# Kernel optimization log

Measured on AMD Instinct MI355X. Metric: run time of the kernel, lower is better.

Reference implementation:

```python
import jax, jax.numpy as jnp
import numpy as np


def conv1x1(x, w, b):
    # x: [B, Cin, H, W], w: [Cout, Cin], b: [Cout]
    return jnp.einsum('oc,bchw->bohw', w, x) + b[None, :, None, None]


def setup_inputs() -> dict:
    key = jax.random.key(0)
    ks = jax.random.split(key, 10)
    B, C, H, W = 8, 256, 64, 64
    C2 = C // 2
    s = 1.0 / np.sqrt(C)
    s2 = 1.0 / np.sqrt(C2)
    return {
        'x1': jax.random.normal(ks[0], (B, C, H, W), jnp.float32),
        'x2': jax.random.normal(ks[1], (B, C, H, W), jnp.float32),
        'w_th': jax.random.uniform(ks[2], (C2, C), jnp.float32, -s, s),
        'b_th': jax.random.uniform(ks[3], (C2,), jnp.float32, -s, s),
        'w_pi': jax.random.uniform(ks[4], (C2, C), jnp.float32, -s, s),
        'b_pi': jax.random.uniform(ks[5], (C2,), jnp.float32, -s, s),
        'w_g': jax.random.uniform(ks[6], (C2, C), jnp.float32, -s, s),
        'b_g': jax.random.uniform(ks[7], (C2,), jnp.float32, -s, s),
        'w_out': jax.random.uniform(ks[8], (C, C2), jnp.float32, -s2, s2),
        'b_out': jax.random.uniform(ks[9], (C,), jnp.float32, -s2, s2),
    }


def reference(x1, x2, w_th, b_th, w_pi, b_pi, w_g, b_g, w_out, b_out):
    B, C, H, W = x1.shape
    HW = H * W
    res = x1
    # 1x1 conv projections -> [B, C2, HW]
    e1 = conv1x1(x1, w_th, b_th).reshape(B, -1, HW)  # theta
    e2 = conv1x1(x2, w_pi, b_pi).reshape(B, -1, HW)  # phi
    # scores: [B, HW, HW]
    f = jnp.einsum('bcq,bck->bqk', e1, e2)
    # GLOBAL softmax over the whole HWxHW matrix per batch element
    f = jax.nn.softmax(f.reshape(B, HW * HW), axis=1).reshape(B, HW, HW)
    g2 = conv1x1(x2, w_g, b_g).reshape(B, -1, HW)  # [B, C2, HW]
    # out = f @ g2^T -> [B, HW, C2] -> [B, C2, H, W]
    out = jnp.einsum('bqk,bck->bcq', f, g2).reshape(B, -1, H, W)
    out = conv1x1(out, w_out, b_out)
    return out + res
```

## Files before the change

kernel.cpp:

```cpp
#include <hip/hip_runtime.h>

typedef unsigned short u16;
typedef unsigned int u32;
typedef short s16x8 __attribute__((ext_vector_type(8)));
typedef float f32x4 __attribute__((ext_vector_type(4)));

#define HWN 4096
#define CC  256
#define C2  128

static __device__ __forceinline__ u16 f2bf(float f) {
    union { float f; u32 u; } c; c.f = f;
    u32 u = c.u;
    u32 r = (u + 0x7fffu + ((u >> 16) & 1u)) >> 16;
    return (u16)r;
}
static __device__ __forceinline__ float bf2f(u16 u) {
    union { u32 u; float f; } c; c.u = ((u32)u) << 16; return c.f;
}
static __device__ __forceinline__ u32 cvtpk(float lo, float hi) {
    u32 d;
    asm("v_cvt_pk_bf16_f32 %0, %1, %2" : "=v"(d) : "v"(lo), "v"(hi));
    return d;
}

__global__ __launch_bounds__(256) void k_wcvt(
    const float* __restrict__ w_th, const float* __restrict__ w_pi,
    const float* __restrict__ w_g,  const float* __restrict__ w_out,
    u16* __restrict__ wthb, u16* __restrict__ wpib,
    u16* __restrict__ wgb,  u16* __restrict__ woutb)
{
    int i = blockIdx.x * 256 + threadIdx.x;
    wthb[i]  = f2bf(w_th[i]);
    wpib[i]  = f2bf(w_pi[i]);
    wgb[i]   = f2bf(w_g[i]);
    woutb[i] = f2bf(w_out[i]);
}

__device__ __forceinline__ void load_afrag(const float* __restrict__ px, int g, s16x8 a[8]) {
    #pragma unroll
    for (int ks = 0; ks < 8; ++ks) {
        union { s16x8 v; u16 u[8]; } c;
        #pragma unroll
        for (int j = 0; j < 8; ++j)
            c.u[j] = f2bf(px[(size_t)(ks*32 + g*8 + j) * HWN]);
        a[ks] = c.v;
    }
}

__device__ __forceinline__ void proj_gemm(const s16x8 a[8], const u16* __restrict__ wb,
                                          const float* __restrict__ bias,
                                          int m16, int g, f32x4 acc[8]) {
    #pragma unroll
    for (int nb = 0; nb < 8; ++nb) {
        float bv = bias[nb*16 + m16];
        acc[nb] = (f32x4){bv, bv, bv, bv};
    }
    #pragma unroll
    for (int ks = 0; ks < 8; ++ks) {
        #pragma unroll
        for (int nb = 0; nb < 8; ++nb) {
            s16x8 bb = *(const s16x8*)&wb[(size_t)(nb*16 + m16)*CC + ks*32 + g*8];
            acc[nb] = __builtin_amdgcn_mfma_f32_16x16x32_bf16(a[ks], bb, acc[nb], 0, 0, 0);
        }
    }
}

__global__ __launch_bounds__(256) void k_projM(
    const float* __restrict__ x1, const float* __restrict__ x2,
    const u16* __restrict__ wthb, const float* __restrict__ b_th,
    const u16* __restrict__ wpib, const float* __restrict__ b_pi,
    const u16* __restrict__ wgb,  const float* __restrict__ b_g,
    u16* __restrict__ e1t, u16* __restrict__ e2t, u16* __restrict__ g2c)
{
    __shared__ u16 gs[C2][72];
    const int tid  = threadIdx.x;
    const int b    = blockIdx.x >> 6;
    const int q0   = (blockIdx.x & 63) * 64;
    const int wid  = __builtin_amdgcn_readfirstlane(tid >> 6);
    const int lane = tid & 63;
    const int m16  = lane & 15;
    const int g    = lane >> 4;

    s16x8 a[8];
    f32x4 acc[8];

    const float* px1 = x1 + (size_t)b*CC*HWN + q0 + wid*16 + m16;
    load_afrag(px1, g, a);
    proj_gemm(a, wthb, b_th, m16, g, acc);
    #pragma unroll
    for (int nb = 0; nb < 8; ++nb)
        #pragma unroll
        for (int r = 0; r < 4; ++r)
            e1t[((size_t)b*HWN + q0 + wid*16 + g*4 + r)*C2 + nb*16 + m16] = f2bf(acc[nb][r]);

    const float* px2 = x2 + (size_t)b*CC*HWN + q0 + wid*16 + m16;
    load_afrag(px2, g, a);
    proj_gemm(a, wpib, b_pi, m16, g, acc);
    #pragma unroll
    for (int nb = 0; nb < 8; ++nb)
        #pragma unroll
        for (int r = 0; r < 4; ++r)
            e2t[((size_t)b*HWN + q0 + wid*16 + g*4 + r)*C2 + nb*16 + m16] = f2bf(acc[nb][r]);

    proj_gemm(a, wgb, b_g, m16, g, acc);
    #pragma unroll
    for (int nb = 0; nb < 8; ++nb)
        #pragma unroll
        for (int r = 0; r < 4; ++r)
            gs[nb*16 + m16][wid*16 + g*4 + r] = f2bf(acc[nb][r]);
    __syncthreads();
    #pragma unroll
    for (int r = 0; r < 4; ++r) {
        int idx = r*256 + tid;
        int c2 = idx >> 3, q8 = idx & 7;
        union { u16 u[8]; int4 v; } o;
        #pragma unroll
        for (int e = 0; e < 8; ++e) {
            int kp = q8*8 + e;
            int kk = kp >> 5, rem = kp & 31;
            int gg = rem >> 3, jj = rem & 7;
            int ko = kk*32 + ((jj >> 2) << 4) + (gg << 2) + (jj & 3);
            o.u[e] = gs[c2][ko];
        }
        *(int4*)&g2c[((size_t)b*C2 + c2)*HWN + q0 + q8*8] = o.v;
    }
}

__global__ __launch_bounds__(256, 2) void k_flash(
    const u16* __restrict__ e1t, const u16* __restrict__ e2t,
    const u16* __restrict__ g2c,
    u16* __restrict__ outp0, u16* __restrict__ outp1, float* __restrict__ ms)
{
    __shared__ u16 e2s[64*128];
    __shared__ u16 g2s[128*64];

    const int tid  = threadIdx.x;
    const int bid  = ((blockIdx.x & 7) << 6) | (blockIdx.x >> 3);
    const int b    = bid >> 6;
    const int qb   = (bid >> 1) & 31;
    const int seg  = bid & 1;
    const int q0   = qb * 128;
    const int wid  = __builtin_amdgcn_readfirstlane(tid >> 6);
    const int lane = tid & 63;
    const int m16  = lane & 15;
    const int g    = lane >> 4;
    const int sw16 = (m16 & 7) << 3;

    s16x8 af[2][4];
    #pragma unroll
    for (int h = 0; h < 2; ++h) {
        const u16* p = e1t + ((size_t)b*HWN + q0 + wid*32 + h*16 + m16)*C2 + g*8;
        #pragma unroll
        for (int kc = 0; kc < 4; ++kc) af[h][kc] = *(const s16x8*)(p + kc*32);
    }

    f32x4 acc[2][8];
    #pragma unroll
    for (int h = 0; h < 2; ++h)
        #pragma unroll
        for (int i = 0; i < 8; ++i) acc[h][i] = (f32x4){0.f,0.f,0.f,0.f};
    float m_w = -INFINITY, s_w = 0.f;

    const u16* e2base = e2t + (size_t)b*HWN*C2;
    const u16* g2base = g2c + (size_t)b*C2*HWN;
    const int er = tid >> 4, ec = tid & 15;
    const int gr = tid >> 3, gc = tid & 7;

    for (int it = 0; it < 32; ++it) {
        const int k0 = seg*2048 + it*64;
        __syncthreads();
        #pragma unroll
        for (int r = 0; r < 4; ++r) {
            int row = r*16 + er;
            int4 v = *(const int4*)(e2base + (size_t)(k0 + row)*C2 + ec*8);
            *(int4*)&e2s[(row*128 + ec*8) ^ ((row & 7) << 3)] = v;
        }
        #pragma unroll
        for (int r = 0; r < 4; ++r) {
            int row = r*32 + gr;
            int4 v = *(const int4*)(g2base + (size_t)row*HWN + k0 + gc*8);
            *(int4*)&g2s[(row*64 + gc*8) ^ ((row & 7) << 3)] = v;
        }
        __syncthreads();

        f32x4 s[2][4];
        #pragma unroll
        for (int h = 0; h < 2; ++h)
            #pragma unroll
            for (int j = 0; j < 4; ++j) s[h][j] = (f32x4){0.f,0.f,0.f,0.f};
        #pragma unroll
        for (int j = 0; j < 4; ++j) {
            #pragma unroll
            for (int kc = 0; kc < 4; ++kc) {
                s16x8 aa = *(const s16x8*)&e2s[((j*16+m16)*128 + kc*32 + g*8) ^ sw16];
                s[0][j] = __builtin_amdgcn_mfma_f32_16x16x32_bf16(aa, af[0][kc], s[0][j], 0, 0, 0);
                s[1][j] = __builtin_amdgcn_mfma_f32_16x16x32_bf16(aa, af[1][kc], s[1][j], 0, 0, 0);
            }
        }

        float tm = -INFINITY;
        #pragma unroll
        for (int h = 0; h < 2; ++h)
            #pragma unroll
            for (int j = 0; j < 4; ++j)
                #pragma unroll
                for (int r = 0; r < 4; ++r) tm = fmaxf(tm, s[h][j][r]);
        #pragma unroll
        for (int off = 32; off >= 1; off >>= 1) tm = fmaxf(tm, __shfl_xor(tm, off));
        if (tm > m_w + 8.f) {
            const float sc = __expf(m_w - tm);
            s_w *= sc;
            #pragma unroll
            for (int h = 0; h < 2; ++h)
                #pragma unroll
                for (int i = 0; i < 8; ++i) {
                    acc[h][i][0] *= sc; acc[h][i][1] *= sc;
                    acc[h][i][2] *= sc; acc[h][i][3] *= sc;
                }
            m_w = tm;
        }
        float psum = 0.f;
        u32 w[2][4][2];
        #pragma unroll
        for (int h = 0; h < 2; ++h)
            #pragma unroll
            for (int j = 0; j < 4; ++j) {
                float p0 = __expf(s[h][j][0] - m_w);
                float p1 = __expf(s[h][j][1] - m_w);
                float p2 = __expf(s[h][j][2] - m_w);
                float p3 = __expf(s[h][j][3] - m_w);
                psum += (p0 + p1) + (p2 + p3);
                w[h][j][0] = cvtpk(p0, p1);
                w[h][j][1] = cvtpk(p2, p3);
            }
        s_w += psum;

        s16x8 pa[2][2];
        #pragma unroll
        for (int h = 0; h < 2; ++h)
            #pragma unroll
            for (int kk = 0; kk < 2; ++kk) {
                union { u32 d[4]; s16x8 v; } pf;
                pf.d[0] = w[h][2*kk][0];
                pf.d[1] = w[h][2*kk][1];
                pf.d[2] = w[h][2*kk+1][0];
                pf.d[3] = w[h][2*kk+1][1];
                pa[h][kk] = pf.v;
            }

        #pragma unroll
        for (int kk = 0; kk < 2; ++kk) {
            #pragma unroll
            for (int fc = 0; fc < 8; ++fc) {
                s16x8 gb = *(const s16x8*)&g2s[((fc*16+m16)*64 + kk*32 + g*8) ^ sw16];
                acc[0][fc] = __builtin_amdgcn_mfma_f32_16x16x32_bf16(pa[0][kk], gb, acc[0][fc], 0, 0, 0);
                acc[1][fc] = __builtin_amdgcn_mfma_f32_16x16x32_bf16(pa[1][kk], gb, acc[1][fc], 0, 0, 0);
            }
        }
    }

    #pragma unroll
    for (int off = 32; off >= 1; off >>= 1) s_w += __shfl_xor(s_w, off);
    if (lane == 0) {
        int idx = b*256 + seg*128 + qb*4 + wid;
        ms[idx*2 + 0] = m_w;
        ms[idx*2 + 1] = s_w;
    }
    const float inv_s = 1.f / s_w;
    u16* op = seg ? outp1 : outp0;
    #pragma unroll
    for (int h = 0; h < 2; ++h)
        #pragma unroll
        for (int fc = 0; fc < 8; ++fc)
            #pragma unroll
            for (int r = 0; r < 4; ++r)
                op[((size_t)b*HWN + q0 + wid*32 + h*16 + g*4 + r)*C2 + fc*16 + m16] =
                    f2bf(acc[h][fc][r] * inv_s);
}

__global__ void k_mz(const float* __restrict__ ms, float* __restrict__ mz)
{
    __shared__ float rmax[4], rsum[4];
    const int b = blockIdx.x, tid = threadIdx.x;
    const int lane = tid & 63, wid = tid >> 6;
    float m = ms[((size_t)b*256 + tid)*2 + 0];
    float s = ms[((size_t)b*256 + tid)*2 + 1];
    float mm = m;
    #pragma unroll
    for (int off = 32; off >= 1; off >>= 1) mm = fmaxf(mm, __shfl_xor(mm, off));
    if (lane == 0) rmax[wid] = mm;
    __syncthreads();
    float M = fmaxf(fmaxf(rmax[0], rmax[1]), fmaxf(rmax[2], rmax[3]));
    float z = s * __expf(m - M);
    #pragma unroll
    for (int off = 32; off >= 1; off >>= 1) z += __shfl_xor(z, off);
    if (lane == 0) rsum[wid] = z;
    __syncthreads();
    if (tid == 0) { mz[b*2] = M; mz[b*2+1] = rsum[0]+rsum[1]+rsum[2]+rsum[3]; }
}

__global__ __launch_bounds__(256) void k_outM(
    const u16* __restrict__ outp0, const u16* __restrict__ outp1,
    const float* __restrict__ ms, const float* __restrict__ mz,
    const u16* __restrict__ woutb, const float* __restrict__ b_out,
    const float* __restrict__ x1, float* __restrict__ out)
{
    const int tid  = threadIdx.x;
    const int b    = blockIdx.x >> 6;
    const int q0   = (blockIdx.x & 63) * 64;
    const int wv   = tid >> 6;
    const int lane = tid & 63;
    const int m16  = lane & 15;
    const int g    = lane >> 4;
    const int q    = q0 + wv*16 + m16;

    const float M    = mz[b*2];
    const float invZ = 1.f / mz[b*2+1];
    const int idx5   = (q0 >> 5) + (wv >> 1);
    const float a0 = ms[(b*256 + idx5)*2+1]       * __expf(ms[(b*256 + idx5)*2]       - M) * invZ;
    const float a1 = ms[(b*256 + 128 + idx5)*2+1] * __expf(ms[(b*256 + 128 + idx5)*2] - M) * invZ;

    s16x8 bfr[4];
    #pragma unroll
    for (int ks = 0; ks < 4; ++ks) {
        union { s16x8 v; u16 u[8]; } o0, o1, oc;
        o0.v = *(const s16x8*)&outp0[((size_t)b*HWN + q)*C2 + ks*32 + g*8];
        o1.v = *(const s16x8*)&outp1[((size_t)b*HWN + q)*C2 + ks*32 + g*8];
        #pragma unroll
        for (int j = 0; j < 8; ++j)
            oc.u[j] = f2bf(a0*bf2f(o0.u[j]) + a1*bf2f(o1.u[j]));
        bfr[ks] = oc.v;
    }

    f32x4 acc[16];
    #pragma unroll
    for (int cb = 0; cb < 16; ++cb) acc[cb] = (f32x4){0.f,0.f,0.f,0.f};
    #pragma unroll
    for (int ks = 0; ks < 4; ++ks) {
        #pragma unroll
        for (int cb = 0; cb < 16; ++cb) {
            s16x8 afr = *(const s16x8*)&woutb[(size_t)(cb*16 + m16)*C2 + ks*32 + g*8];
            acc[cb] = __builtin_amdgcn_mfma_f32_16x16x32_bf16(afr, bfr[ks], acc[cb], 0, 0, 0);
        }
    }

    #pragma unroll
    for (int cb = 0; cb < 16; ++cb) {
        f32x4 bb = *(const f32x4*)&b_out[cb*16 + g*4];
        #pragma unroll
        for (int r = 0; r < 4; ++r) {
            int co = cb*16 + g*4 + r;
            size_t o = ((size_t)b*CC + co)*HWN + q;
            out[o] = acc[cb][r] + bb[r] + x1[o];
        }
    }
}

extern "C" void kernel_launch(void* const* d_in, const int* in_sizes, int n_in,
                              void* d_out, int out_size, void* d_ws, size_t ws_size,
                              hipStream_t stream)
{
    const float* x1   = (const float*)d_in[0];
    const float* x2   = (const float*)d_in[1];
    const float* w_th = (const float*)d_in[2];
    const float* b_th = (const float*)d_in[3];
    const float* w_pi = (const float*)d_in[4];
    const float* b_pi = (const float*)d_in[5];
    const float* w_g  = (const float*)d_in[6];
    const float* b_g  = (const float*)d_in[7];
    const float* w_out= (const float*)d_in[8];
    const float* b_out= (const float*)d_in[9];
    float* out = (float*)d_out;

    char* ws = (char*)d_ws;
    u16*   e1t  = (u16*)(ws);
    u16*   e2t  = (u16*)(ws + 8388608);
    u16*   g2c  = (u16*)(ws + 16777216);
    u16*   outp0= (u16*)(ws + 25165824);
    u16*   outp1= (u16*)(ws + 33554432);
    float* ms   = (float*)(ws + 41943040);
    float* mz   = (float*)(ws + 41959424);
    u16*   wthb = (u16*)(ws + 41959488);
    u16*   wpib = (u16*)(ws + 42025024);
    u16*   wgb  = (u16*)(ws + 42090560);
    u16*   woutb= (u16*)(ws + 42156096);

    k_wcvt <<<dim3(128), dim3(256), 0, stream>>>(w_th, w_pi, w_g, w_out, wthb, wpib, wgb, woutb);
    k_projM<<<dim3(512), dim3(256), 0, stream>>>(x1, x2, wthb, b_th, wpib, b_pi, wgb, b_g,
                                                 e1t, e2t, g2c);
    k_flash<<<dim3(512), dim3(256), 0, stream>>>(e1t, e2t, g2c, outp0, outp1, ms);
    k_mz   <<<dim3(8),   dim3(256), 0, stream>>>(ms, mz);
    k_outM <<<dim3(512), dim3(256), 0, stream>>>(outp0, outp1, ms, mz, woutb, b_out, x1, out);
}
```

Baseline: 182.1 us.

## Double-buffer flash tiles via direct global-to-LDS loads with pre-swizzled layouts

The projection kernel now writes e2 and g2 in a pre-swizzled, tile-contiguous layout. This lets the flash kernel fetch each 64-key tile with global_load_lds straight into LDS, double-buffered so the next tile loads while the current one is computed. It also folds log2(e) into the theta weights and bias so the softmax can use exp2f instead of exp. In exchange it doubles LDS usage per block, which may limit occupancy at two blocks per CU, and it ties the flash kernel to the new layout.

```diff
diff --git a/kernel.cpp b/kernel.cpp
--- a/kernel.cpp
+++ b/kernel.cpp
@@ -8,6 +8,7 @@
 #define HWN 4096
 #define CC  256
 #define C2  128
+#define LOG2E 1.4426950408889634f
 
 static __device__ __forceinline__ u16 f2bf(float f) {
     union { float f; u32 u; } c; c.f = f;
@@ -23,6 +24,8 @@
     asm("v_cvt_pk_bf16_f32 %0, %1, %2" : "=v"(d) : "v"(lo), "v"(hi));
     return d;
 }
+#define GLB(p) ((const __attribute__((address_space(1))) void*)(p))
+#define LDS(p) ((__attribute__((address_space(3))) void*)(p))
 
 __global__ __launch_bounds__(256) void k_wcvt(
     const float* __restrict__ w_th, const float* __restrict__ w_pi,
@@ -31,7 +34,7 @@
     u16* __restrict__ wgb,  u16* __restrict__ woutb)
 {
     int i = blockIdx.x * 256 + threadIdx.x;
-    wthb[i]  = f2bf(w_th[i]);
+    wthb[i]  = f2bf(w_th[i] * LOG2E);
     wpib[i]  = f2bf(w_pi[i]);
     wgb[i]   = f2bf(w_g[i]);
     woutb[i] = f2bf(w_out[i]);
@@ -49,11 +52,11 @@
 }
 
 __device__ __forceinline__ void proj_gemm(const s16x8 a[8], const u16* __restrict__ wb,
-                                          const float* __restrict__ bias,
+                                          const float* __restrict__ bias, float bscale,
                                           int m16, int g, f32x4 acc[8]) {
     #pragma unroll
     for (int nb = 0; nb < 8; ++nb) {
-        float bv = bias[nb*16 + m16];
+        float bv = bias[nb*16 + m16] * bscale;
         acc[nb] = (f32x4){bv, bv, bv, bv};
     }
     #pragma unroll
@@ -71,7 +74,7 @@
     const u16* __restrict__ wthb, const float* __restrict__ b_th,
     const u16* __restrict__ wpib, const float* __restrict__ b_pi,
     const u16* __restrict__ wgb,  const float* __restrict__ b_g,
-    u16* __restrict__ e1t, u16* __restrict__ e2t, u16* __restrict__ g2c)
+    u16* __restrict__ e1t, u16* __restrict__ e2t, u16* __restrict__ g2t)
 {
     __shared__ u16 gs[C2][72];
     const int tid  = threadIdx.x;
@@ -87,7 +90,7 @@
 
     const float* px1 = x1 + (size_t)b*CC*HWN + q0 + wid*16 + m16;
     load_afrag(px1, g, a);
-    proj_gemm(a, wthb, b_th, m16, g, acc);
+    proj_gemm(a, wthb, b_th, LOG2E, m16, g, acc);
     #pragma unroll
     for (int nb = 0; nb < 8; ++nb)
         #pragma unroll
@@ -96,44 +99,49 @@
 
     const float* px2 = x2 + (size_t)b*CC*HWN + q0 + wid*16 + m16;
     load_afrag(px2, g, a);
-    proj_gemm(a, wpib, b_pi, m16, g, acc);
+    proj_gemm(a, wpib, b_pi, 1.f, m16, g, acc);
     #pragma unroll
     for (int nb = 0; nb < 8; ++nb)
         #pragma unroll
-        for (int r = 0; r < 4; ++r)
-            e2t[((size_t)b*HWN + q0 + wid*16 + g*4 + r)*C2 + nb*16 + m16] = f2bf(acc[nb][r]);
-
-    proj_gemm(a, wgb, b_g, m16, g, acc);
+        for (int r = 0; r < 4; ++r) {
+            int q   = q0 + wid*16 + g*4 + r;
+            int gix = (nb*2 + (m16 >> 3)) ^ (q & 7);
+            e2t[((size_t)b*HWN + q)*C2 + gix*8 + (m16 & 7)] = f2bf(acc[nb][r]);
+        }
+
+    proj_gemm(a, wgb, b_g, 1.f, m16, g, acc);
     #pragma unroll
     for (int nb = 0; nb < 8; ++nb)
         #pragma unroll
         for (int r = 0; r < 4; ++r)
             gs[nb*16 + m16][wid*16 + g*4 + r] = f2bf(acc[nb][r]);
     __syncthreads();
+    u16* gt = g2t + ((size_t)b*64 + (q0 >> 6))*8192;
     #pragma unroll
     for (int r = 0; r < 4; ++r) {
         int idx = r*256 + tid;
-        int c2 = idx >> 3, q8 = idx & 7;
+        int row = idx >> 3, c8 = idx & 7;
         union { u16 u[8]; int4 v; } o;
         #pragma unroll
         for (int e = 0; e < 8; ++e) {
-            int kp = q8*8 + e;
-            int kk = kp >> 5, rem = kp & 31;
+            int c  = c8*8 + e;
+            int cs = c ^ ((row & 7) << 3);
+            int kk = cs >> 5, rem = cs & 31;
             int gg = rem >> 3, jj = rem & 7;
             int ko = kk*32 + ((jj >> 2) << 4) + (gg << 2) + (jj & 3);
-            o.u[e] = gs[c2][ko];
-        }
-        *(int4*)&g2c[((size_t)b*C2 + c2)*HWN + q0 + q8*8] = o.v;
+            o.u[e] = gs[row][ko];
+        }
+        *(int4*)&gt[row*64 + c8*8] = o.v;
     }
 }
 
 __global__ __launch_bounds__(256, 2) void k_flash(
     const u16* __restrict__ e1t, const u16* __restrict__ e2t,
-    const u16* __restrict__ g2c,
+    const u16* __restrict__ g2t,
     u16* __restrict__ outp0, u16* __restrict__ outp1, float* __restrict__ ms)
 {
-    __shared__ u16 e2s[64*128];
-    __shared__ u16 g2s[128*64];
+    __shared__ u16 e2s[2][64*128];
+    __shared__ u16 g2s[2][128*64];
 
     const int tid  = threadIdx.x;
     const int bid  = ((blockIdx.x & 7) << 6) | (blockIdx.x >> 3);
@@ -163,26 +171,37 @@
     float m_w = -INFINITY, s_w = 0.f;
 
     const u16* e2base = e2t + (size_t)b*HWN*C2;
-    const u16* g2base = g2c + (size_t)b*C2*HWN;
-    const int er = tid >> 4, ec = tid & 15;
-    const int gr = tid >> 3, gc = tid & 7;
+    const u16* g2base = g2t + (size_t)b*64*8192;
+    const int  wof    = wid * 2048;
+    const int  lof    = lane * 8;
+
+    {
+        const u16* eG = e2base + (size_t)(seg*2048)*C2 + wof + lof;
+        const u16* gG = g2base + (size_t)(seg*32)*8192 + wof + lof;
+        u16* eL = &e2s[0][0] + wof;
+        u16* gL = &g2s[0][0] + wof;
+        #pragma unroll
+        for (int c = 0; c < 4; ++c) {
+            __builtin_amdgcn_global_load_lds(GLB(eG + c*512), LDS(eL + c*512), 16, 0, 0);
+            __builtin_amdgcn_global_load_lds(GLB(gG + c*512), LDS(gL + c*512), 16, 0, 0);
+        }
+    }
+    __syncthreads();
 
     for (int it = 0; it < 32; ++it) {
-        const int k0 = seg*2048 + it*64;
-        __syncthreads();
-        #pragma unroll
-        for (int r = 0; r < 4; ++r) {
-            int row = r*16 + er;
-            int4 v = *(const int4*)(e2base + (size_t)(k0 + row)*C2 + ec*8);
-            *(int4*)&e2s[(row*128 + ec*8) ^ ((row & 7) << 3)] = v;
-        }
-        #pragma unroll
-        for (int r = 0; r < 4; ++r) {
-            int row = r*32 + gr;
-            int4 v = *(const int4*)(g2base + (size_t)row*HWN + k0 + gc*8);
-            *(int4*)&g2s[(row*64 + gc*8) ^ ((row & 7) << 3)] = v;
-        }
-        __syncthreads();
+        const int cur = it & 1;
+        if (it + 1 < 32) {
+            const int k0n = seg*2048 + (it+1)*64;
+            const u16* eG = e2base + (size_t)k0n*C2 + wof + lof;
+            const u16* gG = g2base + (size_t)(k0n >> 6)*8192 + wof + lof;
+            u16* eL = &e2s[cur ^ 1][0] + wof;
+            u16* gL = &g2s[cur ^ 1][0] + wof;
+            #pragma unroll
+            for (int c = 0; c < 4; ++c) {
+                __builtin_amdgcn_global_load_lds(GLB(eG + c*512), LDS(eL + c*512), 16, 0, 0);
+                __builtin_amdgcn_global_load_lds(GLB(gG + c*512), LDS(gL + c*512), 16, 0, 0);
+            }
+        }
 
         f32x4 s[2][4];
         #pragma unroll
@@ -193,7 +212,7 @@
         for (int j = 0; j < 4; ++j) {
             #pragma unroll
             for (int kc = 0; kc < 4; ++kc) {
-                s16x8 aa = *(const s16x8*)&e2s[((j*16+m16)*128 + kc*32 + g*8) ^ sw16];
+                s16x8 aa = *(const s16x8*)&e2s[cur][((j*16+m16)*128 + kc*32 + g*8) ^ sw16];
                 s[0][j] = __builtin_amdgcn_mfma_f32_16x16x32_bf16(aa, af[0][kc], s[0][j], 0, 0, 0);
                 s[1][j] = __builtin_amdgcn_mfma_f32_16x16x32_bf16(aa, af[1][kc], s[1][j], 0, 0, 0);
             }
@@ -208,8 +227,8 @@
                 for (int r = 0; r < 4; ++r) tm = fmaxf(tm, s[h][j][r]);
         #pragma unroll
         for (int off = 32; off >= 1; off >>= 1) tm = fmaxf(tm, __shfl_xor(tm, off));
-        if (tm > m_w + 8.f) {
-            const float sc = __expf(m_w - tm);
+        if (tm > m_w + 11.5416f) {
+            const float sc = exp2f(m_w - tm);
             s_w *= sc;
             #pragma unroll
             for (int h = 0; h < 2; ++h)
@@ -226,10 +245,10 @@
         for (int h = 0; h < 2; ++h)
             #pragma unroll
             for (int j = 0; j < 4; ++j) {
-                float p0 = __expf(s[h][j][0] - m_w);
-                float p1 = __expf(s[h][j][1] - m_w);
-                float p2 = __expf(s[h][j][2] - m_w);
-                float p3 = __expf(s[h][j][3] - m_w);
+                float p0 = exp2f(s[h][j][0] - m_w);
+                float p1 = exp2f(s[h][j][1] - m_w);
+                float p2 = exp2f(s[h][j][2] - m_w);
+                float p3 = exp2f(s[h][j][3] - m_w);
                 psum += (p0 + p1) + (p2 + p3);
                 w[h][j][0] = cvtpk(p0, p1);
                 w[h][j][1] = cvtpk(p2, p3);
@@ -253,11 +272,13 @@
         for (int kk = 0; kk < 2; ++kk) {
             #pragma unroll
             for (int fc = 0; fc < 8; ++fc) {
-                s16x8 gb = *(const s16x8*)&g2s[((fc*16+m16)*64 + kk*32 + g*8) ^ sw16];
+                s16x8 gb = *(const s16x8*)&g2s[cur][((fc*16+m16)*64 + kk*32 + g*8) ^ sw16];
                 acc[0][fc] = __builtin_amdgcn_mfma_f32_16x16x32_bf16(pa[0][kk], gb, acc[0][fc], 0, 0, 0);
                 acc[1][fc] = __builtin_amdgcn_mfma_f32_16x16x32_bf16(pa[1][kk], gb, acc[1][fc], 0, 0, 0);
             }
         }
+
+        __syncthreads();
     }
 
     #pragma unroll
@@ -292,7 +313,7 @@
     if (lane == 0) rmax[wid] = mm;
     __syncthreads();
     float M = fmaxf(fmaxf(rmax[0], rmax[1]), fmaxf(rmax[2], rmax[3]));
-    float z = s * __expf(m - M);
+    float z = s * exp2f(m - M);
     #pragma unroll
     for (int off = 32; off >= 1; off >>= 1) z += __shfl_xor(z, off);
     if (lane == 0) rsum[wid] = z;
@@ -318,8 +339,8 @@
     const float M    = mz[b*2];
     const float invZ = 1.f / mz[b*2+1];
     const int idx5   = (q0 >> 5) + (wv >> 1);
-    const float a0 = ms[(b*256 + idx5)*2+1]       * __expf(ms[(b*256 + idx5)*2]       - M) * invZ;
-    const float a1 = ms[(b*256 + 128 + idx5)*2+1] * __expf(ms[(b*256 + 128 + idx5)*2] - M) * invZ;
+    const float a0 = ms[(b*256 + idx5)*2+1]       * exp2f(ms[(b*256 + idx5)*2]       - M) * invZ;
+    const float a1 = ms[(b*256 + 128 + idx5)*2+1] * exp2f(ms[(b*256 + 128 + idx5)*2] - M) * invZ;
 
     s16x8 bfr[4];
     #pragma unroll
@@ -376,7 +397,7 @@
     char* ws = (char*)d_ws;
     u16*   e1t  = (u16*)(ws);
     u16*   e2t  = (u16*)(ws + 8388608);
-    u16*   g2c  = (u16*)(ws + 16777216);
+    u16*   g2t  = (u16*)(ws + 16777216);
     u16*   outp0= (u16*)(ws + 25165824);
     u16*   outp1= (u16*)(ws + 33554432);
     float* ms   = (float*)(ws + 41943040);
@@ -388,8 +409,8 @@
 
     k_wcvt <<<dim3(128), dim3(256), 0, stream>>>(w_th, w_pi, w_g, w_out, wthb, wpib, wgb, woutb);
     k_projM<<<dim3(512), dim3(256), 0, stream>>>(x1, x2, wthb, b_th, wpib, b_pi, wgb, b_g,
-                                                 e1t, e2t, g2c);
-    k_flash<<<dim3(512), dim3(256), 0, stream>>>(e1t, e2t, g2c, outp0, outp1, ms);
+                                                 e1t, e2t, g2t);
+    k_flash<<<dim3(512), dim3(256), 0, stream>>>(e1t, e2t, g2t, outp0, outp1, ms);
     k_mz   <<<dim3(8),   dim3(256), 0, stream>>>(ms, mz);
     k_outM <<<dim3(512), dim3(256), 0, stream>>>(outp0, outp1, ms, mz, woutb, b_out, x1, out);
 }
```

Measured after the change: 198.0 us. 1.09x slower.
